# Kernel optimization log

Measured on AMD Instinct MI355X. Metric: run time of the kernel, lower is better.

## Reference

```python
import jax, jax.numpy as jnp
import numpy as np

N_NODES = 50000

def sage_conv(x, src, dst, W_l, b_l, W_r):
    # mean-aggregate neighbor features x[src] at dst, then lin_l(agg)+lin_r(x)
    msgs = x[src]                                       # [E, d]
    agg = jax.ops.segment_sum(msgs, dst, num_segments=N_NODES)
    cnt = jax.ops.segment_sum(jnp.ones((src.shape[0],), x.dtype), dst, num_segments=N_NODES)
    agg = agg / jnp.maximum(cnt, 1.0)[:, None]          # [N, d]
    return agg @ W_l.T + b_l + x @ W_r.T


def setup_inputs() -> dict:
    key = jax.random.key(0)
    ks = jax.random.split(key, 10)
    in_c, hid, out_c = 128, 128, 64
    x = jax.random.normal(ks[0], (N_NODES, in_c), dtype=jnp.float32)
    edge_index = jax.random.randint(ks[1], (2, 800000), 0, N_NODES, dtype=jnp.int64)
    s = 1.0 / np.sqrt(in_c)
    W1_l = jax.random.uniform(ks[2], (hid, in_c), minval=-s, maxval=s)
    b1 = jax.random.uniform(ks[3], (hid,), minval=-s, maxval=s)
    W1_r = jax.random.uniform(ks[4], (hid, in_c), minval=-s, maxval=s)
    s = 1.0 / np.sqrt(hid)
    W2_l = jax.random.uniform(ks[5], (hid, hid), minval=-s, maxval=s)
    b2 = jax.random.uniform(ks[6], (hid,), minval=-s, maxval=s)
    W2_r = jax.random.uniform(ks[7], (hid, hid), minval=-s, maxval=s)
    W3 = jax.random.uniform(ks[8], (out_c, hid), minval=-s, maxval=s)
    b3 = jax.random.uniform(ks[9], (out_c,), minval=-s, maxval=s)
    return {"x": x, "edge_index": edge_index, "W1_l": W1_l, "b1": b1, "W1_r": W1_r,
            "W2_l": W2_l, "b2": b2, "W2_r": W2_r, "W3": W3, "b3": b3}


def reference(x, edge_index, W1_l, b1, W1_r, W2_l, b2, W2_r, W3, b3):
    src, dst = edge_index[0], edge_index[1]
    h = jax.nn.relu(sage_conv(x, src, dst, W1_l, b1, W1_r))
    h = jax.nn.relu(sage_conv(h, src, dst, W2_l, b2, W2_r))
    return h @ W3.T + b3
```

## Files before the change

### kernel.cpp

```cpp
#include <hip/hip_runtime.h>

#define FDIM 128

typedef __attribute__((ext_vector_type(8))) short bf16x8;
typedef __attribute__((ext_vector_type(4))) float f32x4;
typedef __attribute__((ext_vector_type(2))) float f32x2;

static __device__ __forceinline__ ushort f2bf(float f) {
    uint u = __float_as_uint(f);
    uint r = (u + 0x7FFF + ((u >> 16) & 1)) >> 16;
    return (ushort)r;
}
static __device__ __forceinline__ uint packbf(float lo, float hi) {
    return (uint)f2bf(lo) | ((uint)f2bf(hi) << 16);
}
static __device__ __forceinline__ uint pk8(float a, float b, float c, float d) {
    uint u = __builtin_amdgcn_cvt_pk_fp8_f32(a, b, 0, false);
    return __builtin_amdgcn_cvt_pk_fp8_f32(c, d, u, true);
}
static __device__ __forceinline__ uchar pk1(float v) {
    return (uchar)(__builtin_amdgcn_cvt_pk_fp8_f32(v, v, 0, false) & 0xFF);
}

#define ACCF8(A, V) do { \
    f32x2 p0 = __builtin_amdgcn_cvt_pk_f32_fp8((V).x, false); \
    f32x2 p1 = __builtin_amdgcn_cvt_pk_f32_fp8((V).x, true);  \
    f32x2 p2 = __builtin_amdgcn_cvt_pk_f32_fp8((V).y, false); \
    f32x2 p3 = __builtin_amdgcn_cvt_pk_f32_fp8((V).y, true);  \
    A[0] += p0.x; A[1] += p0.y; A[2] += p1.x; A[3] += p1.y;   \
    A[4] += p2.x; A[5] += p2.y; A[6] += p3.x; A[7] += p3.y; } while (0)


__global__ void prep_kernel(const float* __restrict__ x, ushort* __restrict__ xbn,
                            uchar* __restrict__ xf8, int nx8,
                            const float* __restrict__ W1l, const float* __restrict__ W1r,
                            const float* __restrict__ W2l, const float* __restrict__ W2r,
                            const float* __restrict__ W3, ushort* __restrict__ wbuf,
                            const int* __restrict__ dst, int E, int* __restrict__ bcnt,
                            int* __restrict__ hdone, int* __restrict__ bbase,
                            int* __restrict__ bcur, int nb, int nconv, int nhist) {
    const int b = blockIdx.x;
    const int tid = threadIdx.x;
    if (b < nconv) {
        int i = b * 256 + tid;
        if (i < nx8) {
            const float* s = x + (size_t)i * 8;
            float4 a = *(const float4*)(s);
            float4 c = *(const float4*)(s + 4);
            uint4 o;
            o.x = packbf(a.x, a.y); o.y = packbf(a.z, a.w);
            o.z = packbf(c.x, c.y); o.w = packbf(c.z, c.w);
            *(uint4*)(xbn + (size_t)i * 8) = o;
            uint2 q;
            q.x = pk8(a.x, a.y, a.z, a.w);
            q.y = pk8(c.x, c.y, c.z, c.w);
            *(uint2*)(xf8 + (size_t)i * 8) = q;
        }
    } else if (b < nconv + 36) {
        int c = (b - nconv) * 256 + tid;
        const float* s; ushort* d;
        if (c < 2048)      { s = W1l + (size_t)c * 8;          d = wbuf + (size_t)c * 8; }
        else if (c < 4096) { s = W1r + (size_t)(c - 2048) * 8; d = wbuf + 16384 + (size_t)(c - 2048) * 8; }
        else if (c < 6144) { s = W2l + (size_t)(c - 4096) * 8; d = wbuf + 32768 + (size_t)(c - 4096) * 8; }
        else if (c < 8192) { s = W2r + (size_t)(c - 6144) * 8; d = wbuf + 49152 + (size_t)(c - 6144) * 8; }
        else               { s = W3  + (size_t)(c - 8192) * 8; d = wbuf + 65536 + (size_t)(c - 8192) * 8; }
        float4 a = *(const float4*)(s);
        float4 cc = *(const float4*)(s + 4);
        uint4 o;
        o.x = packbf(a.x, a.y); o.y = packbf(a.z, a.w);
        o.z = packbf(cc.x, cc.y); o.w = packbf(cc.z, cc.w);
        *(uint4*)d = o;
    } else {
        __shared__ int lh[256];
        __shared__ int isLast;
        int hb = b - nconv - 36;
        lh[tid] = 0;
        __syncthreads();
        #pragma unroll
        for (int k = 0; k < 8; ++k) {
            int e = hb * 2048 + k * 256 + tid;
            if (e < E) atomicAdd(&lh[dst[e] >> 8], 1);
        }
        __syncthreads();
        if (lh[tid]) atomicAdd(&bcnt[tid], lh[tid]);
        __syncthreads();
        if (tid == 0) {
            __threadfence();
            isLast = (atomicAdd(hdone, 1) == nhist - 1);
        }
        __syncthreads();
        if (isLast && tid < 64) {
            __threadfence();
            volatile int* vb = bcnt;
            const int i0 = tid * 4;
            int v0 = (i0 + 0 < nb) ? vb[i0 + 0] : 0;
            int v1 = (i0 + 1 < nb) ? vb[i0 + 1] : 0;
            int v2 = (i0 + 2 < nb) ? vb[i0 + 2] : 0;
            int v3 = (i0 + 3 < nb) ? vb[i0 + 3] : 0;
            int s = v0 + v1 + v2 + v3;
            int incl = s;
            #pragma unroll
            for (int d = 1; d < 64; d <<= 1) {
                int t = __shfl_up(incl, d);
                if (tid >= d) incl += t;
            }
            int excl = incl - s;
            int e0 = excl, e1 = excl + v0, e2 = e1 + v1, e3 = e2 + v2;
            if (i0 + 0 < nb) { bbase[i0 + 0] = e0; bcur[i0 + 0] = e0; }
            if (i0 + 1 < nb) { bbase[i0 + 1] = e1; bcur[i0 + 1] = e1; }
            if (i0 + 2 < nb) { bbase[i0 + 2] = e2; bcur[i0 + 2] = e2; }
            if (i0 + 3 < nb) { bbase[i0 + 3] = e3; bcur[i0 + 3] = e3; }
            int total = __shfl(incl, 63);
            if (tid == 0) bbase[nb] = total;
        }
    }
}


__global__ void pair_scatter(const int* __restrict__ src, const int* __restrict__ dst,
                             int* __restrict__ bcur, uint* __restrict__ pairs, int E) {
    __shared__ int lh[256];
    __shared__ int gb[256];
    const int tid = threadIdx.x;
    lh[tid] = 0;
    __syncthreads();
    int ss[8], dd[8], sl[8];
    #pragma unroll
    for (int k = 0; k < 8; ++k) {
        int e = blockIdx.x * 2048 + k * 256 + tid;
        if (e < E) {
            ss[k] = src[e];
            dd[k] = dst[e];
            sl[k] = atomicAdd(&lh[dd[k] >> 8], 1);
        } else dd[k] = -1;
    }
    __syncthreads();
    if (lh[tid]) gb[tid] = atomicAdd(&bcur[tid], lh[tid]);
    __syncthreads();
    #pragma unroll
    for (int k = 0; k < 8; ++k) {
        if (dd[k] >= 0)
            pairs[gb[dd[k] >> 8] + sl[k]] = (uint)ss[k] | ((uint)(dd[k] & 255) << 24);
    }
}


__global__ void bucket_csr(const uint* __restrict__ pairs, const int* __restrict__ bbase,
                           int* __restrict__ off, int* __restrict__ csr, int N) {
    __shared__ int cnt[256];
    __shared__ int base[256];
    __shared__ int cur[256];
    const int b = blockIdx.x;
    const int tid = threadIdx.x;
    const int p0 = bbase[b], p1 = bbase[b + 1];
    cnt[tid] = 0;
    __syncthreads();
    for (int p = p0 + tid; p < p1; p += 256) atomicAdd(&cnt[pairs[p] >> 24], 1);
    __syncthreads();
    if (tid < 64) {
        int i0 = tid * 4;
        int v0 = cnt[i0], v1 = cnt[i0 + 1], v2 = cnt[i0 + 2], v3 = cnt[i0 + 3];
        int s = v0 + v1 + v2 + v3;
        int incl = s;
        #pragma unroll
        for (int d = 1; d < 64; d <<= 1) {
            int t = __shfl_up(incl, d);
            if (tid >= d) incl += t;
        }
        int excl = incl - s;
        base[i0] = excl; base[i0 + 1] = excl + v0;
        base[i0 + 2] = excl + v0 + v1; base[i0 + 3] = excl + v0 + v1 + v2;
        cur[i0] = base[i0]; cur[i0 + 1] = base[i0 + 1];
        cur[i0 + 2] = base[i0 + 2]; cur[i0 + 3] = base[i0 + 3];
    }
    __syncthreads();
    int node = (b << 8) + tid;
    if (node <= N) off[node] = p0 + base[tid];
    for (int p = p0 + tid; p < p1; p += 256) {
        uint e = pairs[p];
        int slot = atomicAdd(&cur[e >> 24], 1);
        csr[p0 + slot] = (int)(e & 0xFFFFFF);
    }
}


#define PS 132

template<int HEAD>
__global__ __launch_bounds__(256, 8)
void fused_sage(const uchar* __restrict__ feat8, const ushort* __restrict__ featn,
                const int* __restrict__ off, const int* __restrict__ csr,
                const ushort* __restrict__ Wl, const ushort* __restrict__ Wr,
                const float* __restrict__ bias,
                const ushort* __restrict__ W3, const float* __restrict__ b3,
                ushort* __restrict__ houtn, uchar* __restrict__ hout8,
                float* __restrict__ fout, int n) {
    __shared__ __align__(16) ushort As[16 * FDIM];
    __shared__ __align__(16) ushort Xs[16 * FDIM];
    __shared__ __align__(16) float psum[16 * PS];
    const int row0 = blockIdx.x * 16;
    const int lane = threadIdx.x & 63;
    const int wid  = threadIdx.x >> 6;

    {
        int r = threadIdx.x >> 4, cch = threadIdx.x & 15;
        int row = row0 + r;
        float4 vx = make_float4(0.f, 0.f, 0.f, 0.f);
        if (row < n) vx = *(const float4*)(featn + (size_t)row * FDIM + cch * 8);
        *(float4*)(Xs + (r * 16 + (cch ^ (r & 7))) * 8) = vx;
    }

    const int g = lane >> 4;
    const int c = lane & 15;
    #define LDROW(s) (*(const uint2*)(feat8 + (size_t)(s) * FDIM + c * 8))
    for (int i = 0; i < 4; ++i) {
        const int r = wid * 4 + i;
        const int node = row0 + r;
        float a[8] = {0.f, 0.f, 0.f, 0.f, 0.f, 0.f, 0.f, 0.f};
        float inv = 0.f;
        if (node < n) {
            const int j0 = off[node], j1 = off[node + 1];
            int j = j0 + g;
            for (; j + 12 < j1; j += 16) {
                int s0 = csr[j], s1 = csr[j + 4], s2 = csr[j + 8], s3 = csr[j + 12];
                uint2 v0 = LDROW(s0), v1 = LDROW(s1), v2 = LDROW(s2), v3 = LDROW(s3);
                ACCF8(a, v0); ACCF8(a, v1); ACCF8(a, v2); ACCF8(a, v3);
            }
            for (; j + 4 < j1; j += 8) {
                int s0 = csr[j], s1 = csr[j + 4];
                uint2 v0 = LDROW(s0), v1 = LDROW(s1);
                ACCF8(a, v0); ACCF8(a, v1);
            }
            for (; j < j1; j += 4) {
                uint2 v0 = LDROW(csr[j]);
                ACCF8(a, v0);
            }
            inv = 1.0f / fmaxf((float)(j1 - j0), 1.0f);
        }
        #pragma unroll
        for (int k = 0; k < 8; ++k) {
            a[k] += __shfl_xor(a[k], 16);
            a[k] += __shfl_xor(a[k], 32);
        }
        if (g == 0) {
            uint4 o;
            o.x = packbf(a[0] * inv, a[1] * inv);
            o.y = packbf(a[2] * inv, a[3] * inv);
            o.z = packbf(a[4] * inv, a[5] * inv);
            o.w = packbf(a[6] * inv, a[7] * inv);
            *(uint4*)(As + (r * 16 + (c ^ (r & 7))) * 8) = o;
        }
    }
    #undef LDROW
    __syncthreads();

    const int op   = wid >> 1;
    const int half = wid & 1;
    const int lr = lane & 15;
    const int lk = lane >> 4;
    const ushort* Atile = op ? Xs : As;
    const ushort* W     = op ? Wr : Wl;

    f32x4 acc[4];
    #pragma unroll
    for (int t = 0; t < 4; ++t) acc[t] = (f32x4){0.f, 0.f, 0.f, 0.f};

    #pragma unroll
    for (int ks = 0; ks < 4; ++ks) {
        bf16x8 a = *(const bf16x8*)(Atile + (lr * 16 + ((ks * 4 + lk) ^ (lr & 7))) * 8);
        #pragma unroll
        for (int t = 0; t < 4; ++t) {
            int wr = half * 64 + t * 16 + lr;
            bf16x8 bb = *(const bf16x8*)(W + (size_t)wr * FDIM + ks * 32 + lk * 8);
            acc[t] = __builtin_amdgcn_mfma_f32_16x16x32_bf16(a, bb, acc[t], 0, 0, 0);
        }
    }

    if (op == 1) {
        #pragma unroll
        for (int t = 0; t < 4; ++t) {
            #pragma unroll
            for (int j = 0; j < 4; ++j)
                psum[(lk * 4 + j) * PS + half * 64 + t * 16 + lr] = acc[t][j];
        }
    }
    __syncthreads();

    if (op == 0) {
        #pragma unroll
        for (int t = 0; t < 4; ++t) {
            int col = half * 64 + t * 16 + lr;
            float bc = bias[col];
            #pragma unroll
            for (int j = 0; j < 4; ++j) {
                int r = lk * 4 + j;
                float v = fmaxf(acc[t][j] + psum[r * PS + col] + bc, 0.f);
                if (HEAD == 0) {
                    int row = row0 + r;
                    if (row < n) {
                        houtn[(size_t)row * FDIM + col] = f2bf(v);
                        hout8[(size_t)row * FDIM + col] = pk1(v);
                    }
                } else {
                    As[(r * 16 + ((col >> 3) ^ (r & 7))) * 8 + (col & 7)] = f2bf(v);
                }
            }
        }
    }

    if (HEAD == 1) {
        __syncthreads();
        f32x4 acc2 = (f32x4){0.f, 0.f, 0.f, 0.f};
        #pragma unroll
        for (int ks = 0; ks < 4; ++ks) {
            bf16x8 a = *(const bf16x8*)(As + (lr * 16 + ((ks * 4 + lk) ^ (lr & 7))) * 8);
            int wr = wid * 16 + lr;
            bf16x8 bb = *(const bf16x8*)(W3 + (size_t)wr * FDIM + ks * 32 + lk * 8);
            acc2 = __builtin_amdgcn_mfma_f32_16x16x32_bf16(a, bb, acc2, 0, 0, 0);
        }
        int col = wid * 16 + lr;
        float bc = b3[col];
        #pragma unroll
        for (int j = 0; j < 4; ++j) {
            int row = row0 + lk * 4 + j;
            if (row < n) fout[(size_t)row * 64 + col] = acc2[j] + bc;
        }
    }
}


extern "C" void kernel_launch(void* const* d_in, const int* in_sizes, int n_in,
                              void* d_out, int out_size, void* d_ws, size_t ws_size,
                              hipStream_t stream) {
    const float* x   = (const float*)d_in[0];
    const int*   ei  = (const int*)d_in[1];
    const float* W1l = (const float*)d_in[2];
    const float* b1  = (const float*)d_in[3];
    const float* W1r = (const float*)d_in[4];
    const float* W2l = (const float*)d_in[5];
    const float* b2  = (const float*)d_in[6];
    const float* W2r = (const float*)d_in[7];
    const float* W3  = (const float*)d_in[8];
    const float* b3  = (const float*)d_in[9];
    float* out = (float*)d_out;

    const int N = in_sizes[0] / FDIM;
    const int E = in_sizes[1] / 2;
    const int* src = ei;
    const int* dst = ei + E;
    const int NBK = (N + 255) >> 8;

    char* ws = (char*)d_ws;
    size_t p = 0;
    auto alloc = [&](size_t bytes) {
        char* q = ws + p;
        p += (bytes + 255) & ~(size_t)255;
        return q;
    };
    int* ctrl    = (int*)alloc(272 * 4);
    int* bcnt    = ctrl;
    int* hdone   = ctrl + 256;
    int* bbase   = (int*)alloc(260 * 4);
    int* bcur    = (int*)alloc(256 * 4);
    uint* pairs  = (uint*)alloc((size_t)E * 4);
    int* csr     = (int*)alloc((size_t)E * 4);
    int* off     = (int*)alloc((size_t)(N + 1) * 4);
    ushort* xbn  = (ushort*)alloc((size_t)N * FDIM * 2);
    uchar*  xf8  = (uchar*)alloc((size_t)N * FDIM);
    ushort* h1n  = (ushort*)alloc((size_t)N * FDIM * 2);
    uchar*  h1f8 = (uchar*)alloc((size_t)N * FDIM);
    ushort* wbuf = (ushort*)alloc(73728 * 2);
    ushort* w1l = wbuf, *w1r = wbuf + 16384, *w2l = wbuf + 32768,
           *w2r = wbuf + 49152, *w3 = wbuf + 65536;

    hipMemsetAsync(ctrl, 0, 257 * 4, stream);

    const int nx8   = N * FDIM / 8;
    const int nconv = (nx8 + 255) / 256;
    const int nhist = (E + 2047) / 2048;
    prep_kernel<<<nconv + 36 + nhist, 256, 0, stream>>>(
        x, xbn, xf8, nx8, W1l, W1r, W2l, W2r, W3, wbuf, dst, E, bcnt,
        hdone, bbase, bcur, NBK, nconv, nhist);
    pair_scatter<<<(E + 2047) / 2048, 256, 0, stream>>>(src, dst, bcur, pairs, E);
    bucket_csr<<<NBK, 256, 0, stream>>>(pairs, bbase, off, csr, N);

    const int lgrid = (N + 15) / 16;
    fused_sage<0><<<lgrid, 256, 0, stream>>>(xf8, xbn, off, csr, w1l, w1r, b1,
                                             (const ushort*)nullptr, (const float*)nullptr,
                                             h1n, h1f8, (float*)nullptr, N);
    fused_sage<1><<<lgrid, 256, 0, stream>>>(h1f8, h1n, off, csr, w2l, w2r, b2,
                                             w3, b3, (ushort*)nullptr, (uchar*)nullptr, out, N);
}
```

Before: 166.0 us.

## Aggregate four nodes per wavefront concurrently with shuffled neighbor indices

```diff
diff --git a/kernel.cpp b/kernel.cpp
--- a/kernel.cpp
+++ b/kernel.cpp
@@ -210,48 +210,38 @@
         *(float4*)(Xs + (r * 16 + (cch ^ (r & 7))) * 8) = vx;
     }
 
-    const int g = lane >> 4;
-    const int c = lane & 15;
-    #define LDROW(s) (*(const uint2*)(feat8 + (size_t)(s) * FDIM + c * 8))
-    for (int i = 0; i < 4; ++i) {
-        const int r = wid * 4 + i;
-        const int node = row0 + r;
+    {
+        const int nsub = lane >> 4;
+        const int c    = lane & 15;
+        const int nodebase = row0 + wid * 4;
+        int offv = off[min(nodebase + min(lane, 4), n)];
+        const int j0  = __shfl(offv, nsub);
+        const int j1  = __shfl(offv, nsub + 1);
+        const int deg = j1 - j0;
+        int md = max(deg, __shfl_xor(deg, 16));
+        md = max(md, __shfl_xor(md, 32));
+
         float a[8] = {0.f, 0.f, 0.f, 0.f, 0.f, 0.f, 0.f, 0.f};
-        float inv = 0.f;
-        if (node < n) {
-            const int j0 = off[node], j1 = off[node + 1];
-            int j = j0 + g;
-            for (; j + 12 < j1; j += 16) {
-                int s0 = csr[j], s1 = csr[j + 4], s2 = csr[j + 8], s3 = csr[j + 12];
-                uint2 v0 = LDROW(s0), v1 = LDROW(s1), v2 = LDROW(s2), v3 = LDROW(s3);
-                ACCF8(a, v0); ACCF8(a, v1); ACCF8(a, v2); ACCF8(a, v3);
+        for (int base = 0; base < md; base += 16) {
+            int idx = (base + c < deg) ? csr[j0 + base + c] : 0;
+            #pragma unroll
+            for (int k = 0; k < 16; ++k) {
+                int s = __shfl(idx, (nsub << 4) | k);
+                if (base + k < deg) {
+                    uint2 v = *(const uint2*)(feat8 + (size_t)s * FDIM + c * 8);
+                    ACCF8(a, v);
+                }
             }
-            for (; j + 4 < j1; j += 8) {
-                int s0 = csr[j], s1 = csr[j + 4];
-                uint2 v0 = LDROW(s0), v1 = LDROW(s1);
-                ACCF8(a, v0); ACCF8(a, v1);
-            }
-            for (; j < j1; j += 4) {
-                uint2 v0 = LDROW(csr[j]);
-                ACCF8(a, v0);
-            }
-            inv = 1.0f / fmaxf((float)(j1 - j0), 1.0f);
-        }
-        #pragma unroll
-        for (int k = 0; k < 8; ++k) {
-            a[k] += __shfl_xor(a[k], 16);
-            a[k] += __shfl_xor(a[k], 32);
-        }
-        if (g == 0) {
-            uint4 o;
-            o.x = packbf(a[0] * inv, a[1] * inv);
-            o.y = packbf(a[2] * inv, a[3] * inv);
-            o.z = packbf(a[4] * inv, a[5] * inv);
-            o.w = packbf(a[6] * inv, a[7] * inv);
-            *(uint4*)(As + (r * 16 + (c ^ (r & 7))) * 8) = o;
-        }
-    }
-    #undef LDROW
+        }
+        float inv = 1.0f / fmaxf((float)deg, 1.0f);
+        const int r = wid * 4 + nsub;
+        uint4 o;
+        o.x = packbf(a[0] * inv, a[1] * inv);
+        o.y = packbf(a[2] * inv, a[3] * inv);
+        o.z = packbf(a[4] * inv, a[5] * inv);
+        o.w = packbf(a[6] * inv, a[7] * inv);
+        *(uint4*)(As + (r * 16 + (c ^ (r & 7))) * 8) = o;
+    }
     __syncthreads();
 
     const int op   = wid >> 1;
```

Result: no change. 163.8 us (-1.4%).
